# Kernel optimization log

Measured on AMD Instinct MI355X. Metric: run time of the kernel, lower is better.

The kernel has to match this reference:

```python
import jax, jax.numpy as jnp
import numpy as np

D_MODEL = 2048
NUM_HEADS = 16
D_K = D_MODEL // NUM_HEADS  # 128
THETA = 10000.0
BATCH = 2
SEQ = 2048


def _rope(v, pos):
    # v: [..., S, d_k], pos: [..., S] int
    half = v.shape[-1] // 2
    inv_freq = THETA ** (-(jnp.arange(half, dtype=jnp.float32) * 2.0) / v.shape[-1])
    ang = pos[..., None].astype(jnp.float32) * inv_freq  # [..., S, half]
    cos, sin = jnp.cos(ang), jnp.sin(ang)
    x1 = v[..., 0::2]
    x2 = v[..., 1::2]
    r1 = x1 * cos - x2 * sin
    r2 = x1 * sin + x2 * cos
    return jnp.stack([r1, r2], axis=-1).reshape(v.shape)


def setup_inputs() -> dict:
    key = jax.random.key(0)
    ks = jax.random.split(key, 5)
    scale = D_MODEL ** -0.5
    x = jax.random.normal(ks[0], (BATCH, SEQ, D_MODEL), dtype=jnp.float32)
    WQ = jax.random.normal(ks[1], (D_MODEL, D_MODEL), dtype=jnp.float32) * scale
    WK = jax.random.normal(ks[2], (D_MODEL, D_MODEL), dtype=jnp.float32) * scale
    WV = jax.random.normal(ks[3], (D_MODEL, D_MODEL), dtype=jnp.float32) * scale
    WO = jax.random.normal(ks[4], (D_MODEL, D_MODEL), dtype=jnp.float32) * scale
    token_positions = jnp.broadcast_to(jnp.arange(SEQ, dtype=jnp.int32), (BATCH, SEQ))
    return {"x": x, "token_positions": token_positions, "WQ": WQ, "WK": WK, "WV": WV, "WO": WO}


def reference(x, token_positions, WQ, WK, WV, WO):
    B, S, _ = x.shape
    split = lambda t: t.reshape(B, S, NUM_HEADS, D_K).transpose(0, 2, 1, 3)  # [B,H,S,d]
    Q = split(x @ WQ.T)
    K = split(x @ WK.T)
    V = split(x @ WV.T)
    pos = token_positions[:, None, :]  # broadcast over heads
    Q = _rope(Q, pos)
    K = _rope(K, pos)
    scores = jnp.einsum('bhqd,bhkd->bhqk', Q, K) / np.sqrt(D_K).astype(np.float32)
    causal = jnp.arange(S)[:, None] >= jnp.arange(S)[None, :]  # [S,S]
    scores = jnp.where(causal, scores, -jnp.inf)
    attn = jax.nn.softmax(scores, axis=-1)
    out = jnp.einsum('bhqk,bhkd->bhqd', attn, V)
    out = out.transpose(0, 2, 1, 3).reshape(B, S, D_MODEL)
    return out @ WO.T
```

## Files before the change

kernel.cpp:

```cpp
#include <hip/hip_runtime.h>

typedef unsigned short ushort;
typedef __attribute__((ext_vector_type(8))) __bf16 bf16x8;
typedef __attribute__((ext_vector_type(8))) ushort ushort8;
typedef __attribute__((ext_vector_type(4))) float f32x4;
typedef __attribute__((ext_vector_type(16))) float f32x16;
typedef __attribute__((ext_vector_type(4))) unsigned u32x4;

#define DM 2048
#define NH 16
#define DK 128
#define BATCH 2
#define SEQ 2048
#define MROWS (BATCH*SEQ)

#define GLDS16(g, l) __builtin_amdgcn_global_load_lds(                         \
    (const __attribute__((address_space(1))) void*)(g),                        \
    (__attribute__((address_space(3))) void*)(l), 16, 0, 0)

__device__ __forceinline__ ushort f2bf(float f) {
  unsigned u = __builtin_bit_cast(unsigned, f);
  u += 0x7fffu + ((u >> 16) & 1u);
  return (ushort)(u >> 16);
}

__device__ __forceinline__ unsigned cvtpk(float lo, float hi) {
  unsigned r;
  asm("v_cvt_pk_bf16_f32 %0, %1, %2" : "=v"(r) : "v"(lo), "v"(hi));
  return r;
}

__global__ __launch_bounds__(256) void cvt_all(const float* __restrict__ x,
                                               const float* __restrict__ w0,
                                               const float* __restrict__ w1,
                                               const float* __restrict__ w2,
                                               const float* __restrict__ w3,
                                               ushort* __restrict__ xb,
                                               ushort* __restrict__ o0,
                                               ushort* __restrict__ o1,
                                               ushort* __restrict__ o2,
                                               ushort* __restrict__ o3) {
  int b = blockIdx.x;
  const float* src;
  ushort* dst;
  int lb;
  if (b < 4096) { src = x; dst = xb; lb = b; }
  else {
    int wsel = (b - 4096) >> 11;
    lb = (b - 4096) & 2047;
    src = (wsel == 0) ? w0 : (wsel == 1) ? w1 : (wsel == 2) ? w2 : w3;
    dst = (wsel == 0) ? o0 : (wsel == 1) ? o1 : (wsel == 2) ? o2 : o3;
  }
  int i = lb * 256 + threadIdx.x;
  const float4* p = (const float4*)src;
  float4 a = p[2 * i], bq = p[2 * i + 1];
  ushort8 o;
  o[0] = f2bf(a.x); o[1] = f2bf(a.y); o[2] = f2bf(a.z); o[3] = f2bf(a.w);
  o[4] = f2bf(bq.x); o[5] = f2bf(bq.y); o[6] = f2bf(bq.z); o[7] = f2bf(bq.w);
  *(ushort8*)(dst + (size_t)8 * i) = o;
}

template <int NW, int NFR, int MODE>
__device__ __forceinline__ void gemmF_body(const ushort* __restrict__ A,
                                           const ushort* __restrict__ B0,
                                           const ushort* __restrict__ B1,
                                           const ushort* __restrict__ B2,
                                           ushort* __restrict__ O0,
                                           ushort* __restrict__ O1,
                                           ushort* __restrict__ O2,
                                           float* __restrict__ ofp,
                                           int row0, int col0) {
  extern __shared__ ushort lds[];
  constexpr int NT = DM / 64;
  constexpr int BUFSZ = 8192 + NW * NFR * 4096;
  const ushort* Bw[3] = {B0, B1, B2};
  ushort* Ow[3] = {O0, O1, O2};
  const int tid = threadIdx.x;
  const int wid = tid >> 6, lane = tid & 63;
  const int l15 = lane & 15, lhi = lane >> 4;
  const int wm = wid >> 2, wn = wid & 3;
  const int swz = l15 & 7;

  f32x4 acc[4][NW * NFR];
  const f32x4 z4 = {0.f, 0.f, 0.f, 0.f};
#pragma unroll
  for (int mq = 0; mq < 4; ++mq)
#pragma unroll
    for (int i = 0; i < NW * NFR; ++i) acc[mq][i] = z4;

  auto stage = [&](int kt, int buf) {
    ushort* dstA = &lds[buf * BUFSZ];
    const ushort* srcA = A + (size_t)row0 * DM + kt * 64;
#pragma unroll
    for (int j = 0; j < 2; ++j) {
      int g = j * 512 + tid;
      int r = g >> 3, c = g & 7;
      GLDS16(srcA + (size_t)r * DM + ((c ^ (r & 7)) * 8),
             &dstA[(j * 512 + wid * 64) * 8]);
    }
#pragma unroll
    for (int w3 = 0; w3 < NW; ++w3) {
      ushort* dstB = &lds[buf * BUFSZ + 8192 + w3 * NFR * 4096];
      const ushort* srcB = Bw[w3] + (size_t)col0 * DM + kt * 64;
#pragma unroll
      for (int j = 0; j < NFR; ++j) {
        int g = j * 512 + tid;
        int r = g >> 3, c = g & 7;
        GLDS16(srcB + (size_t)r * DM + ((c ^ (r & 7)) * 8),
               &dstB[(j * 512 + wid * 64) * 8]);
      }
    }
  };

  stage(0, 0);
  stage(1, 1);

  for (int t = 0; t < NT; ++t) {
    if (t + 1 < NT) {
      if constexpr (NW == 3)
        asm volatile("s_waitcnt vmcnt(8)" ::: "memory");
      else
        asm volatile("s_waitcnt vmcnt(6)" ::: "memory");
    } else {
      asm volatile("s_waitcnt vmcnt(0)" ::: "memory");
    }
    __builtin_amdgcn_s_barrier();

    const int cb = t & 1;
    const ushort* Ab = &lds[cb * BUFSZ];
    const ushort* Bb = Ab + 8192;
#pragma unroll
    for (int ks = 0; ks < 2; ++ks) {
      bf16x8 af[4];
#pragma unroll
      for (int mq = 0; mq < 4; ++mq) {
        int row = wm * 64 + mq * 16 + l15;
        af[mq] = *(const bf16x8*)&Ab[row * 64 + (((ks * 4 + lhi) ^ swz) * 8)];
      }
      bf16x8 bfr[NW * NFR];
#pragma unroll
      for (int w3 = 0; w3 < NW; ++w3)
#pragma unroll
        for (int n = 0; n < NFR; ++n) {
          int row = wn * (NFR * 16) + n * 16 + l15;
          bfr[w3 * NFR + n] =
              *(const bf16x8*)&Bb[w3 * NFR * 4096 + row * 64 + (((ks * 4 + lhi) ^ swz) * 8)];
        }
      __builtin_amdgcn_s_setprio(1);
#pragma unroll
      for (int mq = 0; mq < 4; ++mq)
#pragma unroll
        for (int i = 0; i < NW * NFR; ++i)
          acc[mq][i] = __builtin_amdgcn_mfma_f32_16x16x32_bf16(af[mq], bfr[i], acc[mq][i], 0, 0, 0);
      __builtin_amdgcn_s_setprio(0);
    }

    __builtin_amdgcn_s_barrier();
    if (t + 2 < NT) stage(t + 2, cb);
  }

#pragma unroll
  for (int mq = 0; mq < 4; ++mq) {
    int grow = row0 + wm * 64 + mq * 16 + lhi * 4;
#pragma unroll
    for (int w3 = 0; w3 < NW; ++w3)
#pragma unroll
      for (int n = 0; n < NFR; ++n) {
        int gcol = col0 + wn * (NFR * 16) + n * 16 + l15;
#pragma unroll
        for (int j = 0; j < 4; ++j) {
          float v = acc[mq][w3 * NFR + n][j];
          int r = grow + j;
          if (MODE == 0) {
            int b = r >> 11, s = r & (SEQ - 1);
            int h = gcol >> 7, d = gcol & (DK - 1);
            Ow[w3][((size_t)(b * NH + h) * SEQ + s) * DK + d] = f2bf(v);
          } else {
            ofp[(size_t)r * DM + gcol] = v;
          }
        }
      }
  }
}

__global__ __launch_bounds__(512, 2) void gemmF_qkv(const ushort* __restrict__ A,
                                                    const ushort* __restrict__ W0,
                                                    const ushort* __restrict__ W1,
                                                    const ushort* __restrict__ W2,
                                                    ushort* __restrict__ O0,
                                                    ushort* __restrict__ O1,
                                                    ushort* __restrict__ O2) {
  int xcd = (int)blockIdx.x & 7, i = (int)blockIdx.x >> 3;
  int row0 = (((xcd >> 2) << 4) + (i >> 2)) * 128;
  int col0 = (((xcd & 3) << 2) + (i & 3)) * 128;
  gemmF_body<3, 2, 0>(A, W0, W1, W2, O0, O1, O2, nullptr, row0, col0);
}

__global__ __launch_bounds__(512, 2) void gemmF_out(const ushort* __restrict__ A,
                                                    const ushort* __restrict__ Bm,
                                                    float* __restrict__ ofp) {
  int xcd = (int)blockIdx.x & 7, i = (int)blockIdx.x >> 3;
  int row0 = (((xcd >> 1) << 3) + (i >> 2)) * 128;
  int col0 = (((xcd & 1) << 2) + (i & 3)) * 256;
  gemmF_body<1, 4, 1>(A, Bm, nullptr, nullptr, nullptr, nullptr, nullptr, ofp, row0, col0);
}

__global__ __launch_bounds__(256) void rope_kernel(ushort* __restrict__ Q,
                                                   ushort* __restrict__ K,
                                                   const int* __restrict__ tpos) {
  int bid = blockIdx.x;
  ushort* buf = (bid & 1) ? K : Q;
  int idx = (bid >> 1) * 256 + threadIdx.x;
  int c = idx & 15;
  int row = idx >> 4;
  int s = row & (SEQ - 1);
  int bh = row >> 11;
  int b = bh >> 4;
  int pos = tpos[b * SEQ + s];
  int d0 = c * 8;
  ushort8 v = *(ushort8*)(buf + (size_t)row * DK + d0);
  float fp = (float)pos;
#pragma unroll
  for (int p = 0; p < 4; ++p) {
    int i = (d0 >> 1) + p;
    float freq = exp2f(-13.287712379549449f * ((float)i * (1.0f / 64.0f)));
    float ang = fp * freq;
    float sn, cs;
    sincosf(ang, &sn, &cs);
    float x1 = __builtin_bit_cast(float, (unsigned)v[2 * p] << 16);
    float x2 = __builtin_bit_cast(float, (unsigned)v[2 * p + 1] << 16);
    float r1 = x1 * cs - x2 * sn;
    float r2 = x1 * sn + x2 * cs;
    v[2 * p] = f2bf(r1);
    v[2 * p + 1] = f2bf(r2);
  }
  *(ushort8*)(buf + (size_t)row * DK + d0) = v;
}

__global__ __launch_bounds__(256) void transpose_v(const ushort* __restrict__ Vb,
                                                   ushort* __restrict__ Vt) {
  __shared__ ushort t[64 * 80];
  int s0 = blockIdx.x * 64, d0 = blockIdx.y * 64, bh = blockIdx.z;
  const size_t base = (size_t)bh * SEQ * DK;
  int tid = threadIdx.x;
#pragma unroll
  for (int it = 0; it < 2; ++it) {
    int c = it * 256 + tid;
    int r = c >> 3, c8 = (c & 7) * 8;
    ushort8 v = *(const ushort8*)&Vb[base + (size_t)(s0 + r) * DK + d0 + c8];
    *(ushort8*)&t[r * 80 + c8] = v;
  }
  __syncthreads();
  const size_t obase = (size_t)bh * DK * SEQ;
#pragma unroll
  for (int it = 0; it < 2; ++it) {
    int c = it * 256 + tid;
    int dr = c >> 3, sc = (c & 7) * 8;
    ushort8 v;
#pragma unroll
    for (int i2 = 0; i2 < 8; ++i2) v[i2] = t[(sc + i2) * 80 + dr];
    *(ushort8*)&Vt[obase + (size_t)(d0 + dr) * SEQ + s0 + sc] = v;
  }
}

__global__ __launch_bounds__(256, 2) void attn_kernel(const ushort* __restrict__ Qb,
                                                      const ushort* __restrict__ Kb,
                                                      const ushort* __restrict__ Vt,
                                                      ushort* __restrict__ attnb) {
  __shared__ ushort lds[32768];
  const int bx = blockIdx.x;
  const int u = bx & 255, hg = bx >> 8;
  const int qt = hg ? (15 - (u & 15)) : (u & 15);
  const int bh = (u >> 4) + hg * 16;
  const int tid = threadIdx.x;
  const int w = tid >> 6, lane = tid & 63;
  const int l31 = lane & 31, hi = lane >> 5;
  const int qb = qt * 128;
  const int qsb = qb + w * 32;
  const int q = qsb + l31;
  const size_t qk_base = (size_t)bh * SEQ * DK;
  const size_t v_base = (size_t)bh * DK * SEQ;
  const int nt = (qb + 128) >> 6;

  bf16x8 qf[8];
#pragma unroll
  for (int ks = 0; ks < 8; ++ks)
    qf[ks] = *(const bf16x8*)&Qb[qk_base + (size_t)q * DK + ks * 16 + hi * 8];

  f32x16 acc[4];
#pragma unroll
  for (int dt = 0; dt < 4; ++dt)
#pragma unroll
    for (int r = 0; r < 16; ++r) acc[dt][r] = 0.f;

  float m2 = -INFINITY, lsum = 0.f;
  const float cs2 = 0.08838834764831845f * 1.4426950408889634f;

  auto stage = [&](int t, int bufsel) {
    const int kb0 = t * 64;
#pragma unroll
    for (int i = 0; i < 4; ++i) {
      int g = w * 256 + i * 64 + lane;
      int row = g >> 4, c16 = g & 15;
      GLDS16(Kb + qk_base + (size_t)(kb0 + row) * DK + ((c16 ^ (row & 7)) * 8),
             &lds[bufsel * 8192 + (w * 256 + i * 64) * 8]);
    }
#pragma unroll
    for (int i = 0; i < 4; ++i) {
      int g = w * 256 + i * 64 + lane;
      int row = g >> 3, c8 = g & 7;
      GLDS16(Vt + v_base + (size_t)row * SEQ + kb0 + ((c8 ^ (row & 7)) * 8),
             &lds[16384 + bufsel * 8192 + (w * 256 + i * 64) * 8]);
    }
  };

  stage(0, 0);
  __syncthreads();
  int buf = 0;

  for (int t = 0; t < nt; ++t) {
    if (t + 1 < nt) stage(t + 1, buf ^ 1);
    const int kb0 = t * 64;
    if (kb0 <= qsb) {
      const ushort* lk = &lds[buf * 8192];
      const ushort* lv = &lds[16384 + buf * 8192];
      const int kb1 = kb0 + 32;
      const bool diag0 = (kb0 == qsb);
      const bool have1 = (kb1 <= qsb);
      const bool diag1 = (kb1 == qsb);
      const int sw = l31 & 7;

      f32x16 s0, s1;
#pragma unroll
      for (int r = 0; r < 16; ++r) { s0[r] = 0.f; s1[r] = 0.f; }
      __builtin_amdgcn_s_setprio(1);
#pragma unroll
      for (int ks = 0; ks < 8; ++ks) {
        int g = 2 * ks + hi;
        bf16x8 kf = *(const bf16x8*)&lk[(l31 * 16 + (g ^ sw)) * 8];
        s0 = __builtin_amdgcn_mfma_f32_32x32x16_bf16(kf, qf[ks], s0, 0, 0, 0);
      }
      if (have1) {
#pragma unroll
        for (int ks = 0; ks < 8; ++ks) {
          int g = 2 * ks + hi;
          bf16x8 kf = *(const bf16x8*)&lk[((32 + l31) * 16 + (g ^ sw)) * 8];
          s1 = __builtin_amdgcn_mfma_f32_32x32x16_bf16(kf, qf[ks], s1, 0, 0, 0);
        }
      }
      __builtin_amdgcn_s_setprio(0);

      float mx = -INFINITY;
#pragma unroll
      for (int r = 0; r < 16; ++r) {
        float v = s0[r] * cs2;
        if (diag0) {
          int kk = kb0 + (r & 3) + 8 * (r >> 2) + 4 * hi;
          if (kk > q) v = -INFINITY;
        }
        s0[r] = v;
        mx = fmaxf(mx, v);
      }
      if (have1) {
#pragma unroll
        for (int r = 0; r < 16; ++r) {
          float v = s1[r] * cs2;
          if (diag1) {
            int kk = kb1 + (r & 3) + 8 * (r >> 2) + 4 * hi;
            if (kk > q) v = -INFINITY;
          }
          s1[r] = v;
          mx = fmaxf(mx, v);
        }
      }
      mx = fmaxf(mx, __shfl_xor(mx, 32));

      float sc = 1.f;
      if (!__all(mx <= m2 + 11.5f)) {
        float mnew = fmaxf(m2, mx);
        sc = exp2f(m2 - mnew);
        m2 = mnew;
#pragma unroll
        for (int dt = 0; dt < 4; ++dt)
#pragma unroll
          for (int r = 0; r < 16; ++r) acc[dt][r] *= sc;
      }
      float rs = 0.f;
#pragma unroll
      for (int r = 0; r < 16; ++r) {
        float p = exp2f(s0[r] - m2);
        s0[r] = p;
        rs += p;
      }
      if (have1) {
#pragma unroll
        for (int r = 0; r < 16; ++r) {
          float p = exp2f(s1[r] - m2);
          s1[r] = p;
          rs += p;
        }
      }
      rs += __shfl_xor(rs, 32);
      lsum = lsum * sc + rs;

      unsigned w0[8], ws0[8];
#pragma unroll
      for (int i = 0; i < 8; ++i) w0[i] = cvtpk(s0[2 * i], s0[2 * i + 1]);
#pragma unroll
      for (int i = 0; i < 8; ++i) ws0[i] = (unsigned)__shfl_xor((int)w0[i], 32);
      u32x4 b00, b01;
      b00[0] = hi ? ws0[2] : w0[0]; b00[1] = hi ? ws0[3] : w0[1];
      b00[2] = hi ? w0[2] : ws0[0]; b00[3] = hi ? w0[3] : ws0[1];
      b01[0] = hi ? ws0[6] : w0[4]; b01[1] = hi ? ws0[7] : w0[5];
      b01[2] = hi ? w0[6] : ws0[4]; b01[3] = hi ? w0[7] : ws0[5];
      bf16x8 pb00 = __builtin_bit_cast(bf16x8, b00);
      bf16x8 pb01 = __builtin_bit_cast(bf16x8, b01);
      bf16x8 pb10, pb11;
      if (have1) {
        unsigned w1[8], ws1[8];
#pragma unroll
        for (int i = 0; i < 8; ++i) w1[i] = cvtpk(s1[2 * i], s1[2 * i + 1]);
#pragma unroll
        for (int i = 0; i < 8; ++i) ws1[i] = (unsigned)__shfl_xor((int)w1[i], 32);
        u32x4 b10, b11;
        b10[0] = hi ? ws1[2] : w1[0]; b10[1] = hi ? ws1[3] : w1[1];
        b10[2] = hi ? w1[2] : ws1[0]; b10[3] = hi ? w1[3] : ws1[1];
        b11[0] = hi ? ws1[6] : w1[4]; b11[1] = hi ? ws1[7] : w1[5];
        b11[2] = hi ? w1[6] : ws1[4]; b11[3] = hi ? w1[7] : ws1[5];
        pb10 = __builtin_bit_cast(bf16x8, b10);
        pb11 = __builtin_bit_cast(bf16x8, b11);
      }

      __builtin_amdgcn_s_setprio(1);
#pragma unroll
      for (int dt = 0; dt < 4; ++dt) {
        int vr = (dt * 32 + l31) * 8;
        bf16x8 vf0 = *(const bf16x8*)&lv[(vr + ((0 + hi) ^ sw)) * 8];
        bf16x8 vf1 = *(const bf16x8*)&lv[(vr + ((2 + hi) ^ sw)) * 8];
        acc[dt] = __builtin_amdgcn_mfma_f32_32x32x16_bf16(vf0, pb00, acc[dt], 0, 0, 0);
        acc[dt] = __builtin_amdgcn_mfma_f32_32x32x16_bf16(vf1, pb01, acc[dt], 0, 0, 0);
        if (have1) {
          bf16x8 vf2 = *(const bf16x8*)&lv[(vr + ((4 + hi) ^ sw)) * 8];
          bf16x8 vf3 = *(const bf16x8*)&lv[(vr + ((6 + hi) ^ sw)) * 8];
          acc[dt] = __builtin_amdgcn_mfma_f32_32x32x16_bf16(vf2, pb10, acc[dt], 0, 0, 0);
          acc[dt] = __builtin_amdgcn_mfma_f32_32x32x16_bf16(vf3, pb11, acc[dt], 0, 0, 0);
        }
      }
      __builtin_amdgcn_s_setprio(0);
    }
    __syncthreads();
    buf ^= 1;
  }

  ushort* eo = &lds[w * 32 * 136];
  float inv = 1.0f / lsum;
#pragma unroll
  for (int dt = 0; dt < 4; ++dt)
#pragma unroll
    for (int rq = 0; rq < 4; ++rq) {
      unsigned lo = cvtpk(acc[dt][4 * rq] * inv, acc[dt][4 * rq + 1] * inv);
      unsigned hh = cvtpk(acc[dt][4 * rq + 2] * inv, acc[dt][4 * rq + 3] * inv);
      uint2 pr; pr.x = lo; pr.y = hh;
      *(uint2*)&eo[l31 * 136 + dt * 32 + rq * 8 + hi * 4] = pr;
    }
  const int b = bh >> 4, h = bh & (NH - 1);
#pragma unroll
  for (int it = 0; it < 8; ++it) {
    int row = it * 4 + (lane >> 4);
    int c8 = (lane & 15) * 8;
    ushort8 v = *(const ushort8*)&eo[row * 136 + c8];
    *(ushort8*)&attnb[((size_t)b * SEQ + qsb + row) * DM + h * DK + c8] = v;
  }
}

extern "C" void kernel_launch(void* const* d_in, const int* in_sizes, int n_in,
                              void* d_out, int out_size, void* d_ws, size_t ws_size,
                              hipStream_t stream) {
  const float* x = (const float*)d_in[0];
  const int* tpos = (const int*)d_in[1];
  const float* WQ = (const float*)d_in[2];
  const float* WK = (const float*)d_in[3];
  const float* WV = (const float*)d_in[4];
  const float* WO = (const float*)d_in[5];
  float* out = (float*)d_out;
  char* ws = (char*)d_ws;

  ushort* xb  = (ushort*)(ws + 0);
  ushort* wqb = (ushort*)(ws + 16777216);
  ushort* wkb = (ushort*)(ws + 25165824);
  ushort* wvb = (ushort*)(ws + 33554432);
  ushort* wob = (ushort*)(ws + 41943040);
  ushort* Qb  = (ushort*)(ws + 50331648);
  ushort* Kb  = (ushort*)(ws + 67108864);
  ushort* Vb  = (ushort*)(ws + 83886080);
  ushort* Vt  = (ushort*)(ws + 0);
  ushort* attnb = (ushort*)(ws + 16777216);

  hipFuncSetAttribute(reinterpret_cast<const void*>(gemmF_qkv),
                      hipFuncAttributeMaxDynamicSharedMemorySize, 131072);
  hipFuncSetAttribute(reinterpret_cast<const void*>(gemmF_out),
                      hipFuncAttributeMaxDynamicSharedMemorySize, 98304);

  cvt_all<<<12288, 256, 0, stream>>>(x, WQ, WK, WV, WO, xb, wqb, wkb, wvb, wob);

  gemmF_qkv<<<512, 512, 131072, stream>>>(xb, wqb, wkb, wvb, Qb, Kb, Vb);

  rope_kernel<<<8192, 256, 0, stream>>>(Qb, Kb, tpos);

  transpose_v<<<dim3(SEQ / 64, DK / 64, BATCH * NH), 256, 0, stream>>>(Vb, Vt);

  attn_kernel<<<dim3(512), 256, 0, stream>>>(Qb, Kb, Vt, attnb);

  gemmF_out<<<256, 512, 98304, stream>>>(attnb, wob, out);
}
```

Measured before the change: 261.7 us.

## Enlarge QKV GEMM row tile to 256 with 8x6 accumulators per wave

The fused QKV projection GEMM now uses 256-row tiles instead of 128, launching 256 blocks instead of 512. Each wave holds 8x6 accumulator fragments, and LDS per block rises to 160 KB. The aim is to reuse each loaded weight tile across twice as many rows, which halves B-matrix traffic and improves MFMA density per LDS read. In exchange it raises register pressure, and the larger LDS footprint likely allows only one block per CU despite the launch bound of 2. The output GEMM is specialized into its own body without behaviour change.

Result: slower. 270.2 us (+3.2%).

```diff
diff --git a/kernel.cpp b/kernel.cpp
--- a/kernel.cpp
+++ b/kernel.cpp
@@ -60,20 +60,20 @@
   *(ushort8*)(dst + (size_t)8 * i) = o;
 }
 
-template <int NW, int NFR, int MODE>
-__device__ __forceinline__ void gemmF_body(const ushort* __restrict__ A,
-                                           const ushort* __restrict__ B0,
-                                           const ushort* __restrict__ B1,
-                                           const ushort* __restrict__ B2,
-                                           ushort* __restrict__ O0,
-                                           ushort* __restrict__ O1,
-                                           ushort* __restrict__ O2,
-                                           float* __restrict__ ofp,
-                                           int row0, int col0) {
+__global__ __launch_bounds__(512, 2) void gemmQ_qkv(const ushort* __restrict__ A,
+                                                    const ushort* __restrict__ W0,
+                                                    const ushort* __restrict__ W1,
+                                                    const ushort* __restrict__ W2,
+                                                    ushort* __restrict__ O0,
+                                                    ushort* __restrict__ O1,
+                                                    ushort* __restrict__ O2) {
   extern __shared__ ushort lds[];
   constexpr int NT = DM / 64;
-  constexpr int BUFSZ = 8192 + NW * NFR * 4096;
-  const ushort* Bw[3] = {B0, B1, B2};
+  constexpr int BUFSZ = 40960;
+  int xcd = (int)blockIdx.x & 7, bi = (int)blockIdx.x >> 3;
+  int row0 = (((xcd >> 2) << 3) + (bi >> 2)) * 256;
+  int col0 = (((xcd & 3) << 2) + (bi & 3)) * 128;
+  const ushort* Bw[3] = {W0, W1, W2};
   ushort* Ow[3] = {O0, O1, O2};
   const int tid = threadIdx.x;
   const int wid = tid >> 6, lane = tid & 63;
@@ -81,12 +81,119 @@
   const int wm = wid >> 2, wn = wid & 3;
   const int swz = l15 & 7;
 
-  f32x4 acc[4][NW * NFR];
+  f32x4 acc[8][6];
   const f32x4 z4 = {0.f, 0.f, 0.f, 0.f};
 #pragma unroll
+  for (int mq = 0; mq < 8; ++mq)
+#pragma unroll
+    for (int i = 0; i < 6; ++i) acc[mq][i] = z4;
+
+  auto stage = [&](int kt, int buf) {
+    ushort* dstA = &lds[buf * BUFSZ];
+    const ushort* srcA = A + (size_t)row0 * DM + kt * 64;
+#pragma unroll
+    for (int j = 0; j < 4; ++j) {
+      int g = j * 512 + tid;
+      int r = g >> 3, c = g & 7;
+      GLDS16(srcA + (size_t)r * DM + ((c ^ (r & 7)) * 8),
+             &dstA[(j * 512 + wid * 64) * 8]);
+    }
+#pragma unroll
+    for (int w3 = 0; w3 < 3; ++w3) {
+      ushort* dstB = &lds[buf * BUFSZ + 16384 + w3 * 8192];
+      const ushort* srcB = Bw[w3] + (size_t)col0 * DM + kt * 64;
+#pragma unroll
+      for (int j = 0; j < 2; ++j) {
+        int g = j * 512 + tid;
+        int r = g >> 3, c = g & 7;
+        GLDS16(srcB + (size_t)r * DM + ((c ^ (r & 7)) * 8),
+               &dstB[(j * 512 + wid * 64) * 8]);
+      }
+    }
+  };
+
+  stage(0, 0);
+  stage(1, 1);
+
+  for (int t = 0; t < NT; ++t) {
+    if (t + 1 < NT)
+      asm volatile("s_waitcnt vmcnt(10)" ::: "memory");
+    else
+      asm volatile("s_waitcnt vmcnt(0)" ::: "memory");
+    __builtin_amdgcn_s_barrier();
+
+    const int cb = t & 1;
+    const ushort* Ab = &lds[cb * BUFSZ];
+    const ushort* Bb = Ab + 16384;
+#pragma unroll
+    for (int ks = 0; ks < 2; ++ks) {
+      bf16x8 af[8];
+#pragma unroll
+      for (int mq = 0; mq < 8; ++mq) {
+        int row = wm * 128 + mq * 16 + l15;
+        af[mq] = *(const bf16x8*)&Ab[row * 64 + (((ks * 4 + lhi) ^ swz) * 8)];
+      }
+#pragma unroll
+      for (int w3 = 0; w3 < 3; ++w3) {
+        bf16x8 bfr[2];
+#pragma unroll
+        for (int n = 0; n < 2; ++n) {
+          int row = wn * 32 + n * 16 + l15;
+          bfr[n] = *(const bf16x8*)&Bb[w3 * 8192 + row * 64 + (((ks * 4 + lhi) ^ swz) * 8)];
+        }
+        __builtin_amdgcn_s_setprio(1);
+#pragma unroll
+        for (int mq = 0; mq < 8; ++mq)
+#pragma unroll
+          for (int n = 0; n < 2; ++n)
+            acc[mq][w3 * 2 + n] = __builtin_amdgcn_mfma_f32_16x16x32_bf16(
+                af[mq], bfr[n], acc[mq][w3 * 2 + n], 0, 0, 0);
+        __builtin_amdgcn_s_setprio(0);
+      }
+    }
+
+    __builtin_amdgcn_s_barrier();
+    if (t + 2 < NT) stage(t + 2, cb);
+  }
+
+#pragma unroll
+  for (int mq = 0; mq < 8; ++mq) {
+    int grow = row0 + wm * 128 + mq * 16 + lhi * 4;
+#pragma unroll
+    for (int w3 = 0; w3 < 3; ++w3)
+#pragma unroll
+      for (int n = 0; n < 2; ++n) {
+        int gcol = col0 + wn * 32 + n * 16 + l15;
+        int h = gcol >> 7, d = gcol & (DK - 1);
+#pragma unroll
+        for (int j = 0; j < 4; ++j) {
+          int r = grow + j;
+          int b = r >> 11, s = r & (SEQ - 1);
+          Ow[w3][((size_t)(b * NH + h) * SEQ + s) * DK + d] = f2bf(acc[mq][w3 * 2 + n][j]);
+        }
+      }
+  }
+}
+
+__device__ __forceinline__ void gemmO_body(const ushort* __restrict__ A,
+                                           const ushort* __restrict__ Bm,
+                                           float* __restrict__ ofp,
+                                           int row0, int col0) {
+  extern __shared__ ushort lds[];
+  constexpr int NT = DM / 64;
+  constexpr int BUFSZ = 8192 + 16384;
+  const int tid = threadIdx.x;
+  const int wid = tid >> 6, lane = tid & 63;
+  const int l15 = lane & 15, lhi = lane >> 4;
+  const int wm = wid >> 2, wn = wid & 3;
+  const int swz = l15 & 7;
+
+  f32x4 acc[4][4];
+  const f32x4 z4 = {0.f, 0.f, 0.f, 0.f};
+#pragma unroll
   for (int mq = 0; mq < 4; ++mq)
 #pragma unroll
-    for (int i = 0; i < NW * NFR; ++i) acc[mq][i] = z4;
+    for (int i = 0; i < 4; ++i) acc[mq][i] = z4;
 
   auto stage = [&](int kt, int buf) {
     ushort* dstA = &lds[buf * BUFSZ];
@@ -98,17 +205,14 @@
       GLDS16(srcA + (size_t)r * DM + ((c ^ (r & 7)) * 8),
              &dstA[(j * 512 + wid * 64) * 8]);
     }
-#pragma unroll
-    for (int w3 = 0; w3 < NW; ++w3) {
-      ushort* dstB = &lds[buf * BUFSZ + 8192 + w3 * NFR * 4096];
-      const ushort* srcB = Bw[w3] + (size_t)col0 * DM + kt * 64;
-#pragma unroll
-      for (int j = 0; j < NFR; ++j) {
-        int g = j * 512 + tid;
-        int r = g >> 3, c = g & 7;
-        GLDS16(srcB + (size_t)r * DM + ((c ^ (r & 7)) * 8),
-               &dstB[(j * 512 + wid * 64) * 8]);
-      }
+    ushort* dstB = &lds[buf * BUFSZ + 8192];
+    const ushort* srcB = Bm + (size_t)col0 * DM + kt * 64;
+#pragma unroll
+    for (int j = 0; j < 4; ++j) {
+      int g = j * 512 + tid;
+      int r = g >> 3, c = g & 7;
+      GLDS16(srcB + (size_t)r * DM + ((c ^ (r & 7)) * 8),
+             &dstB[(j * 512 + wid * 64) * 8]);
     }
   };
 
@@ -116,14 +220,10 @@
   stage(1, 1);
 
   for (int t = 0; t < NT; ++t) {
-    if (t + 1 < NT) {
-      if constexpr (NW == 3)
-        asm volatile("s_waitcnt vmcnt(8)" ::: "memory");
-      else
-        asm volatile("s_waitcnt vmcnt(6)" ::: "memory");
-    } else {
+    if (t + 1 < NT)
+      asm volatile("s_waitcnt vmcnt(6)" ::: "memory");
+    else
       asm volatile("s_waitcnt vmcnt(0)" ::: "memory");
-    }
     __builtin_amdgcn_s_barrier();
 
     const int cb = t & 1;
@@ -137,21 +237,18 @@
         int row = wm * 64 + mq * 16 + l15;
         af[mq] = *(const bf16x8*)&Ab[row * 64 + (((ks * 4 + lhi) ^ swz) * 8)];
       }
-      bf16x8 bfr[NW * NFR];
-#pragma unroll
-      for (int w3 = 0; w3 < NW; ++w3)
-#pragma unroll
-        for (int n = 0; n < NFR; ++n) {
-          int row = wn * (NFR * 16) + n * 16 + l15;
-          bfr[w3 * NFR + n] =
-              *(const bf16x8*)&Bb[w3 * NFR * 4096 + row * 64 + (((ks * 4 + lhi) ^ swz) * 8)];
-        }
+      bf16x8 bfr[4];
+#pragma unroll
+      for (int n = 0; n < 4; ++n) {
+        int row = wn * 64 + n * 16 + l15;
+        bfr[n] = *(const bf16x8*)&Bb[row * 64 + (((ks * 4 + lhi) ^ swz) * 8)];
+      }
       __builtin_amdgcn_s_setprio(1);
 #pragma unroll
       for (int mq = 0; mq < 4; ++mq)
 #pragma unroll
-        for (int i = 0; i < NW * NFR; ++i)
-          acc[mq][i] = __builtin_amdgcn_mfma_f32_16x16x32_bf16(af[mq], bfr[i], acc[mq][i], 0, 0, 0);
+        for (int n = 0; n < 4; ++n)
+          acc[mq][n] = __builtin_amdgcn_mfma_f32_16x16x32_bf16(af[mq], bfr[n], acc[mq][n], 0, 0, 0);
       __builtin_amdgcn_s_setprio(0);
     }
 
@@ -163,37 +260,13 @@
   for (int mq = 0; mq < 4; ++mq) {
     int grow = row0 + wm * 64 + mq * 16 + lhi * 4;
 #pragma unroll
-    for (int w3 = 0; w3 < NW; ++w3)
-#pragma unroll
-      for (int n = 0; n < NFR; ++n) {
-        int gcol = col0 + wn * (NFR * 16) + n * 16 + l15;
-#pragma unroll
-        for (int j = 0; j < 4; ++j) {
-          float v = acc[mq][w3 * NFR + n][j];
-          int r = grow + j;
-          if (MODE == 0) {
-            int b = r >> 11, s = r & (SEQ - 1);
-            int h = gcol >> 7, d = gcol & (DK - 1);
-            Ow[w3][((size_t)(b * NH + h) * SEQ + s) * DK + d] = f2bf(v);
-          } else {
-            ofp[(size_t)r * DM + gcol] = v;
-          }
-        }
-      }
-  }
-}
-
-__global__ __launch_bounds__(512, 2) void gemmF_qkv(const ushort* __restrict__ A,
-                                                    const ushort* __restrict__ W0,
-                                                    const ushort* __restrict__ W1,
-                                                    const ushort* __restrict__ W2,
-                                                    ushort* __restrict__ O0,
-                                                    ushort* __restrict__ O1,
-                                                    ushort* __restrict__ O2) {
-  int xcd = (int)blockIdx.x & 7, i = (int)blockIdx.x >> 3;
-  int row0 = (((xcd >> 2) << 4) + (i >> 2)) * 128;
-  int col0 = (((xcd & 3) << 2) + (i & 3)) * 128;
-  gemmF_body<3, 2, 0>(A, W0, W1, W2, O0, O1, O2, nullptr, row0, col0);
+    for (int n = 0; n < 4; ++n) {
+      int gcol = col0 + wn * 64 + n * 16 + l15;
+#pragma unroll
+      for (int j = 0; j < 4; ++j)
+        ofp[(size_t)(grow + j) * DM + gcol] = acc[mq][n][j];
+    }
+  }
 }
 
 __global__ __launch_bounds__(512, 2) void gemmF_out(const ushort* __restrict__ A,
@@ -202,7 +275,7 @@
   int xcd = (int)blockIdx.x & 7, i = (int)blockIdx.x >> 3;
   int row0 = (((xcd >> 1) << 3) + (i >> 2)) * 128;
   int col0 = (((xcd & 1) << 2) + (i & 3)) * 256;
-  gemmF_body<1, 4, 1>(A, Bm, nullptr, nullptr, nullptr, nullptr, nullptr, ofp, row0, col0);
+  gemmO_body(A, Bm, ofp, row0, col0);
 }
 
 __global__ __launch_bounds__(256) void rope_kernel(ushort* __restrict__ Q,
@@ -496,14 +569,14 @@
   ushort* Vt  = (ushort*)(ws + 0);
   ushort* attnb = (ushort*)(ws + 16777216);
 
-  hipFuncSetAttribute(reinterpret_cast<const void*>(gemmF_qkv),
-                      hipFuncAttributeMaxDynamicSharedMemorySize, 131072);
+  hipFuncSetAttribute(reinterpret_cast<const void*>(gemmQ_qkv),
+                      hipFuncAttributeMaxDynamicSharedMemorySize, 163840);
   hipFuncSetAttribute(reinterpret_cast<const void*>(gemmF_out),
                       hipFuncAttributeMaxDynamicSharedMemorySize, 98304);
 
   cvt_all<<<12288, 256, 0, stream>>>(x, WQ, WK, WV, WO, xb, wqb, wkb, wvb, wob);
 
-  gemmF_qkv<<<512, 512, 131072, stream>>>(xb, wqb, wkb, wvb, Qb, Kb, Vb);
+  gemmQ_qkv<<<256, 512, 163840, stream>>>(xb, wqb, wkb, wvb, Qb, Kb, Vb);
 
   rope_kernel<<<8192, 256, 0, stream>>>(Qb, Kb, tpos);
 
```
